# Optimization experiments

Hardware: AMD Instinct MI355X
Metric: run time of the kernel (lower is better)

The kernel has to match this reference:

```python
import jax, jax.numpy as jnp
import numpy as np

IN_F, OUT_F, GROUP = 4096, 4096, 128
N_GROUPS = IN_F // GROUP  # 32


def setup_inputs() -> dict:
    key = jax.random.key(0)
    k1, k2, k3, k4, k5 = jax.random.split(key, 5)
    x = jax.random.normal(k1, (2, 1024, IN_F), dtype=jnp.float32)
    w_q = jax.random.randint(k2, (OUT_F, N_GROUPS, GROUP), -128, 128, dtype=jnp.int32)  # int8-range quantized weights
    s_w = jax.random.uniform(k3, (N_GROUPS, OUT_F), dtype=jnp.float32) * 0.01  # per-group, per-out-channel scales
    perm = jax.random.permutation(k4, IN_F).astype(jnp.int64)  # GPTQ activation-order permutation
    bias = jax.random.normal(k5, (OUT_F,), dtype=jnp.float32)
    return {"x": x, "w_q": w_q, "s_w": s_w, "perm": perm, "bias": bias}


def reference(x, w_q, s_w, perm, bias):
    prefix = x.shape[:-1]
    orig_dtype = x.dtype
    xf = x.reshape(-1, IN_F)          # (n, in)
    xf = xf[:, perm]                  # apply GPTQ permutation
    xf = xf.reshape(-1, N_GROUPS, GROUP).astype(jnp.float32)  # (n, g, k)
    wf = w_q.astype(jnp.float32)      # (o, g, k) dequant-to-fp32 weights (pre-scale)
    y_g = jnp.einsum('ngk,ogk->ngo', xf, wf)   # per-group partial products (n, g, o)
    y = jnp.sum(y_g * s_w[None, :, :], axis=1) # apply group scales, reduce groups -> (n, o)
    y = y + bias.astype(y.dtype)
    return y.reshape(*prefix, OUT_F).astype(orig_dtype)
```

## Files before the change

kernel.cpp:

```cpp
#include <hip/hip_runtime.h>
#include <hip/hip_bf16.h>
#include <stdint.h>

#define IN_F   4096
#define OUT_F  4096
#define M_ROWS 2048
#define NG     32
#define GRP    128

typedef int   v4i  __attribute__((ext_vector_type(4)));
typedef float f32x4 __attribute__((ext_vector_type(4)));

typedef const void __attribute__((address_space(1))) cv_g;
typedef void       __attribute__((address_space(3))) v_l;

__device__ __forceinline__ void async16(const void* g, void* l) {
  __builtin_amdgcn_global_load_lds((cv_g*)g, (v_l*)l, 16, 0, 0);
}

__device__ int g_perm_is64;

__global__ void decode_flag(const void* __restrict__ perm_raw) {
  if (threadIdx.x == 0 && blockIdx.x == 0) {
    const int* w = (const int*)perm_raw;
    int ok = 1;
    for (int j = 0; j < 32; ++j) {
      int lo = w[2 * j], hi = w[2 * j + 1];
      if (hi != 0 || lo < 0 || lo >= IN_F) { ok = 0; break; }
    }
    g_perm_is64 = ok;
  }
}

__global__ __launch_bounds__(256) void prep(const float* __restrict__ x,
                                            const int* __restrict__ w_q,
                                            const void* __restrict__ perm_raw,
                                            char* __restrict__ xq,
                                            char* __restrict__ w8,
                                            float* __restrict__ sxr) {
  __shared__ float sx[IN_F];
  __shared__ float red[4];
  __shared__ int sflag;
  const int b = blockIdx.x;
  const int t = threadIdx.x;

  if (b < M_ROWS) {
    const int m = b;
    const float* xr = x + (size_t)m * IN_F;
#pragma unroll
    for (int u = 0; u < 4; ++u) {
      int idx = (u * 256 + t) * 4;
      *(float4*)&sx[idx] = *(const float4*)&xr[idx];
    }
    if (t < 64) {
      const int* w = (const int*)perm_raw;
      int j = t & 31;
      int lo = w[2 * j], hi = w[2 * j + 1];
      int cond = (hi == 0 && lo >= 0 && lo < IN_F);
      unsigned long long bal = __ballot(cond);
      if (t == 0) sflag = (bal == ~0ull) ? 1 : 0;
    }
    __syncthreads();
    const int f = sflag;
    const long long* p64 = (const long long*)perm_raw;
    const int*       p32 = (const int*)perm_raw;
    const int jb = t * 16;
    float vals[16];
    float lmax = 0.f;
#pragma unroll
    for (int u = 0; u < 16; ++u) {
      int pj = f ? (int)p64[jb + u] : p32[jb + u];
      float v = sx[pj];
      vals[u] = v;
      lmax = fmaxf(lmax, fabsf(v));
    }
#pragma unroll
    for (int d = 1; d < 64; d <<= 1)
      lmax = fmaxf(lmax, __shfl_xor(lmax, d, 64));
    if ((t & 63) == 0) red[t >> 6] = lmax;
    __syncthreads();
    float rmax = fmaxf(fmaxf(red[0], red[1]), fmaxf(red[2], red[3]));
    float inv = (rmax > 0.f) ? 127.f / rmax : 0.f;
    if (t == 0) sxr[m] = rmax / 127.f;
    char q[16] __attribute__((aligned(16)));
#pragma unroll
    for (int u = 0; u < 16; ++u)
      q[u] = (char)__float2int_rn(vals[u] * inv);
    *(uint4*)(xq + (size_t)m * IN_F + jb) = *(const uint4*)q;
  } else {
    const int o  = b - M_ROWS;
    const int kb = t * 16;
    const int* wr = w_q + (size_t)o * IN_F + kb;
    int4 w0 = *(const int4*)(wr + 0);
    int4 w1 = *(const int4*)(wr + 4);
    int4 w2 = *(const int4*)(wr + 8);
    int4 w3 = *(const int4*)(wr + 12);
    char q[16] __attribute__((aligned(16)));
    q[0]=(char)w0.x; q[1]=(char)w0.y; q[2]=(char)w0.z; q[3]=(char)w0.w;
    q[4]=(char)w1.x; q[5]=(char)w1.y; q[6]=(char)w1.z; q[7]=(char)w1.w;
    q[8]=(char)w2.x; q[9]=(char)w2.y; q[10]=(char)w2.z; q[11]=(char)w2.w;
    q[12]=(char)w3.x; q[13]=(char)w3.y; q[14]=(char)w3.z; q[15]=(char)w3.w;
    *(uint4*)(w8 + (size_t)o * IN_F + kb) = *(const uint4*)q;
  }
}

__global__ __launch_bounds__(256, 2) void gemm_i8(
    const char* __restrict__ A,
    const char* __restrict__ B,
    const float* __restrict__ s_w,
    const float* __restrict__ sxr,
    const float* __restrict__ bias,
    float* __restrict__ C) {
  __shared__ __attribute__((aligned(16))) char lds[73728];
  unsigned short* sws = (unsigned short*)lds;
  const int BUF0 = 8192, BUF1 = 40960;

  const int tid  = threadIdx.x;
  const int wave = tid >> 6;
  const int lane = tid & 63;
  const int bm = blockIdx.y << 7;
  const int bn = blockIdx.x << 7;
  const int wm = (wave >> 1) << 6;
  const int wn = (wave & 1) << 6;
  const int lrow = lane & 15;
  const int quad = lane >> 4;

#pragma unroll
  for (int u = 0; u < 16; ++u) {
    int idx = u * 256 + tid;
    int g = idx >> 7, c = idx & 127;
    __hip_bfloat16 h = __float2bfloat16(s_w[(size_t)g * OUT_F + bn + c]);
    sws[idx] = *(unsigned short*)&h;
  }

  const char* gp[8];
  int lofs[8];
#pragma unroll
  for (int h = 0; h < 8; ++h) {
    int c0 = (h * 4 + wave) * 64;
    int c  = c0 + lane;
    if (c0 < 1024) {
      int row = c >> 3;
      int kc  = (c & 7) ^ (row & 7);
      gp[h]   = A + (size_t)(bm + row) * IN_F + kc * 16;
      lofs[h] = c0 * 16;
    } else {
      int cb  = c - 1024;
      int row = cb >> 3;
      int kc  = (cb & 7) ^ (row & 7);
      gp[h]   = B + (size_t)(bn + row) * IN_F + kc * 16;
      lofs[h] = 16384 + (c0 - 1024) * 16;
    }
  }

  const int xlo = lrow & 7;
  int aoff[2][4], boff[2][4];
#pragma unroll
  for (int s = 0; s < 2; ++s) {
    int slot = (((s << 2) | quad) ^ xlo) << 4;
#pragma unroll
    for (int i = 0; i < 4; ++i) aoff[s][i] = (wm + i * 16 + lrow) * 128 + slot;
#pragma unroll
    for (int j = 0; j < 4; ++j) boff[s][j] = 16384 + (wn + j * 16 + lrow) * 128 + slot;
  }

  f32x4 accf[4][4] = {};
  v4i   acci[4][4] = {};

  auto rescale = [&](int g) {
    float swv[4];
#pragma unroll
    for (int j = 0; j < 4; ++j) {
      unsigned int u = sws[g * 128 + wn + j * 16 + lrow];
      swv[j] = __uint_as_float(u << 16);
    }
#pragma unroll
    for (int i = 0; i < 4; ++i)
#pragma unroll
      for (int j = 0; j < 4; ++j) {
#pragma unroll
        for (int r = 0; r < 4; ++r)
          accf[i][j][r] += swv[j] * (float)acci[i][j][r];
        acci[i][j] = (v4i){0, 0, 0, 0};
      }
  };

  auto tile = [&](int t, int pbase, int qbase, bool doPrev, bool doStage) {
    v4i af0[4], bf0[4], af1[4], bf1[4];
#pragma unroll
    for (int i = 0; i < 4; ++i) af0[i] = *(const v4i*)&lds[pbase + aoff[0][i]];
#pragma unroll
    for (int j = 0; j < 4; ++j) bf0[j] = *(const v4i*)&lds[pbase + boff[0][j]];
#pragma unroll
    for (int i = 0; i < 4; ++i) af1[i] = *(const v4i*)&lds[pbase + aoff[1][i]];
#pragma unroll
    for (int j = 0; j < 4; ++j) bf1[j] = *(const v4i*)&lds[pbase + boff[1][j]];
    if (doStage) {
      const int kn = (t + 1) * GRP;
#pragma unroll
      for (int h = 0; h < 8; ++h) async16(gp[h] + kn, &lds[qbase + lofs[h]]);
    }
    if (doPrev) rescale(t - 1);
    __builtin_amdgcn_s_setprio(1);
#pragma unroll
    for (int i = 0; i < 4; ++i)
#pragma unroll
      for (int j = 0; j < 4; ++j)
        acci[i][j] = __builtin_amdgcn_mfma_i32_16x16x64_i8(af0[i], bf0[j], acci[i][j], 0, 0, 0);
#pragma unroll
    for (int i = 0; i < 4; ++i)
#pragma unroll
      for (int j = 0; j < 4; ++j)
        acci[i][j] = __builtin_amdgcn_mfma_i32_16x16x64_i8(af1[i], bf1[j], acci[i][j], 0, 0, 0);
    __builtin_amdgcn_s_setprio(0);
    if (doStage) asm volatile("s_waitcnt vmcnt(0)" ::: "memory");
    __builtin_amdgcn_s_barrier();
    asm volatile("" ::: "memory");
  };

#pragma unroll
  for (int h = 0; h < 8; ++h) async16(gp[h], &lds[BUF0 + lofs[h]]);
  asm volatile("s_waitcnt vmcnt(0) lgkmcnt(0)" ::: "memory");
  __builtin_amdgcn_s_barrier();
  asm volatile("" ::: "memory");

  for (int it = 0; it < 16; ++it) {
    tile(2 * it,     BUF0, BUF1, it > 0, true);
    tile(2 * it + 1, BUF1, BUF0, true,   it < 15);
  }
  rescale(NG - 1);

#pragma unroll
  for (int i = 0; i < 4; ++i) {
    int r0 = bm + wm + i * 16 + quad * 4;
    float sxv[4];
#pragma unroll
    for (int r = 0; r < 4; ++r) sxv[r] = sxr[r0 + r];
#pragma unroll
    for (int j = 0; j < 4; ++j) {
      int col = bn + wn + j * 16 + lrow;
      float bv = bias[col];
#pragma unroll
      for (int r = 0; r < 4; ++r)
        C[(size_t)(r0 + r) * OUT_F + col] = sxv[r] * accf[i][j][r] + bv;
    }
  }
}

__global__ void naive_fallback(const float* __restrict__ x, const int* __restrict__ w_q,
                               const float* __restrict__ s_w, const void* __restrict__ perm_raw,
                               const float* __restrict__ bias, float* __restrict__ out) {
  int t = blockIdx.x * blockDim.x + threadIdx.x;
  int m = t >> 12;
  int o = t & 4095;
  const int f = g_perm_is64;
  const long long* p64 = (const long long*)perm_raw;
  const int*       p32 = (const int*)perm_raw;
  const float* xr = x + (size_t)m * IN_F;
  const int*   wr = w_q + (size_t)o * IN_F;
  float acc = 0.f;
  for (int g = 0; g < NG; ++g) {
    float part = 0.f;
    for (int k = 0; k < GRP; ++k) {
      int j = g * GRP + k;
      int pj = f ? (int)p64[j] : p32[j];
      part += xr[pj] * (float)wr[j];
    }
    acc += part * s_w[(size_t)g * OUT_F + o];
  }
  out[t] = acc + bias[o];
}

extern "C" void kernel_launch(void* const* d_in, const int* in_sizes, int n_in,
                              void* d_out, int out_size, void* d_ws, size_t ws_size,
                              hipStream_t stream) {
  const float* x    = (const float*)d_in[0];
  const int*   w_q  = (const int*)d_in[1];
  const float* s_w  = (const float*)d_in[2];
  const void*  perm = d_in[3];
  const float* bias = (const float*)d_in[4];
  float* out = (float*)d_out;

  const size_t xq_bytes = (size_t)M_ROWS * IN_F;
  const size_t w8_bytes = (size_t)OUT_F * IN_F;
  const size_t sx_bytes = (size_t)M_ROWS * sizeof(float);
  const size_t need = xq_bytes + w8_bytes + sx_bytes;

  if (ws_size < need) {
    decode_flag<<<1, 64, 0, stream>>>(perm);
    naive_fallback<<<(M_ROWS * OUT_F) / 256, 256, 0, stream>>>(x, w_q, s_w, perm, bias, out);
    return;
  }

  char*  xq  = (char*)d_ws;
  char*  w8  = (char*)d_ws + xq_bytes;
  float* sxr = (float*)((char*)d_ws + xq_bytes + w8_bytes);

  prep<<<M_ROWS + OUT_F, 256, 0, stream>>>(x, w_q, perm, xq, w8, sxr);

  dim3 grid(OUT_F / 128, M_ROWS / 128);
  gemm_i8<<<grid, 256, 0, stream>>>(xq, w8, s_w, sxr, bias, out);
}
```

Baseline: 212.5 us.

## Load A fragments directly from global into registers, stage only B in LDS

The int8 activation (A) tile is no longer staged through LDS. Each wave loads its A MFMA fragments straight from global memory into registers, software-pipelined half a group ahead. Only the weight (B) tile stays double-buffered in LDS, which shrinks LDS use from 72KB to 40KB and could allow more resident blocks. The group rescale is folded right after each group's MFMAs, with no deferred previous-group rescale. The cost is that each A row is now fetched once per wave column (duplicated global/L2 traffic across the two waves sharing rows) and global load latency sits on the critical path. The vmcnt(4) waits are also more delicate.

```diff
diff --git a/kernel.cpp b/kernel.cpp
--- a/kernel.cpp
+++ b/kernel.cpp
@@ -111,9 +111,9 @@
     const float* __restrict__ sxr,
     const float* __restrict__ bias,
     float* __restrict__ C) {
-  __shared__ __attribute__((aligned(16))) char lds[73728];
+  __shared__ __attribute__((aligned(16))) char lds[40960];
   unsigned short* sws = (unsigned short*)lds;
-  const int BUF0 = 8192, BUF1 = 40960;
+  const int BUF0 = 8192, BUF1 = 24576;
 
   const int tid  = threadIdx.x;
   const int wave = tid >> 6;
@@ -124,6 +124,7 @@
   const int wn = (wave & 1) << 6;
   const int lrow = lane & 15;
   const int quad = lane >> 4;
+  const int xlo  = lrow & 7;
 
 #pragma unroll
   for (int u = 0; u < 16; ++u) {
@@ -133,102 +134,106 @@
     sws[idx] = *(unsigned short*)&h;
   }
 
-  const char* gp[8];
-  int lofs[8];
-#pragma unroll
-  for (int h = 0; h < 8; ++h) {
-    int c0 = (h * 4 + wave) * 64;
-    int c  = c0 + lane;
-    if (c0 < 1024) {
-      int row = c >> 3;
-      int kc  = (c & 7) ^ (row & 7);
-      gp[h]   = A + (size_t)(bm + row) * IN_F + kc * 16;
-      lofs[h] = c0 * 16;
-    } else {
-      int cb  = c - 1024;
-      int row = cb >> 3;
-      int kc  = (cb & 7) ^ (row & 7);
-      gp[h]   = B + (size_t)(bn + row) * IN_F + kc * 16;
-      lofs[h] = 16384 + (c0 - 1024) * 16;
-    }
-  }
-
-  const int xlo = lrow & 7;
-  int aoff[2][4], boff[2][4];
-#pragma unroll
-  for (int s = 0; s < 2; ++s) {
-    int slot = (((s << 2) | quad) ^ xlo) << 4;
-#pragma unroll
-    for (int i = 0; i < 4; ++i) aoff[s][i] = (wm + i * 16 + lrow) * 128 + slot;
-#pragma unroll
-    for (int j = 0; j < 4; ++j) boff[s][j] = 16384 + (wn + j * 16 + lrow) * 128 + slot;
-  }
+  const char* gB = B + (size_t)(bn + wave * 8 + (lane >> 3)) * IN_F +
+                   (((lane & 7) ^ (lane >> 3)) << 4);
+  const int lB = wave * 1024;
+
+  const char* gA = A + (size_t)(bm + wm + lrow) * IN_F + (quad << 4);
 
   f32x4 accf[4][4] = {};
-  v4i   acci[4][4] = {};
-
-  auto rescale = [&](int g) {
-    float swv[4];
-#pragma unroll
-    for (int j = 0; j < 4; ++j) {
-      unsigned int u = sws[g * 128 + wn + j * 16 + lrow];
-      swv[j] = __uint_as_float(u << 16);
-    }
-#pragma unroll
-    for (int i = 0; i < 4; ++i)
-#pragma unroll
-      for (int j = 0; j < 4; ++j) {
-#pragma unroll
-        for (int r = 0; r < 4; ++r)
-          accf[i][j][r] += swv[j] * (float)acci[i][j][r];
-        acci[i][j] = (v4i){0, 0, 0, 0};
-      }
-  };
-
-  auto tile = [&](int t, int pbase, int qbase, bool doPrev, bool doStage) {
-    v4i af0[4], bf0[4], af1[4], bf1[4];
-#pragma unroll
-    for (int i = 0; i < 4; ++i) af0[i] = *(const v4i*)&lds[pbase + aoff[0][i]];
-#pragma unroll
-    for (int j = 0; j < 4; ++j) bf0[j] = *(const v4i*)&lds[pbase + boff[0][j]];
-#pragma unroll
-    for (int i = 0; i < 4; ++i) af1[i] = *(const v4i*)&lds[pbase + aoff[1][i]];
-#pragma unroll
-    for (int j = 0; j < 4; ++j) bf1[j] = *(const v4i*)&lds[pbase + boff[1][j]];
-    if (doStage) {
-      const int kn = (t + 1) * GRP;
-#pragma unroll
-      for (int h = 0; h < 8; ++h) async16(gp[h] + kn, &lds[qbase + lofs[h]]);
-    }
-    if (doPrev) rescale(t - 1);
-    __builtin_amdgcn_s_setprio(1);
-#pragma unroll
-    for (int i = 0; i < 4; ++i)
-#pragma unroll
-      for (int j = 0; j < 4; ++j)
-        acci[i][j] = __builtin_amdgcn_mfma_i32_16x16x64_i8(af0[i], bf0[j], acci[i][j], 0, 0, 0);
-#pragma unroll
-    for (int i = 0; i < 4; ++i)
-#pragma unroll
-      for (int j = 0; j < 4; ++j)
-        acci[i][j] = __builtin_amdgcn_mfma_i32_16x16x64_i8(af1[i], bf1[j], acci[i][j], 0, 0, 0);
-    __builtin_amdgcn_s_setprio(0);
-    if (doStage) asm volatile("s_waitcnt vmcnt(0)" ::: "memory");
-    __builtin_amdgcn_s_barrier();
-    asm volatile("" ::: "memory");
-  };
-
-#pragma unroll
-  for (int h = 0; h < 8; ++h) async16(gp[h], &lds[BUF0 + lofs[h]]);
-  asm volatile("s_waitcnt vmcnt(0) lgkmcnt(0)" ::: "memory");
+  const v4i zero4 = {0, 0, 0, 0};
+
+#pragma unroll
+  for (int h = 0; h < 4; ++h)
+    async16(gB + (size_t)h * (32 * IN_F), &lds[BUF0 + lB + h * 4096]);
+  __builtin_amdgcn_sched_barrier(0);
+  v4i afC[4], afN[4];
+#pragma unroll
+  for (int i = 0; i < 4; ++i)
+    afC[i] = *(const v4i*)(gA + (size_t)i * (16 * IN_F));
+  asm volatile("s_waitcnt vmcnt(4) lgkmcnt(0)" ::: "memory");
   __builtin_amdgcn_s_barrier();
   asm volatile("" ::: "memory");
 
-  for (int it = 0; it < 16; ++it) {
-    tile(2 * it,     BUF0, BUF1, it > 0, true);
-    tile(2 * it + 1, BUF1, BUF0, true,   it < 15);
-  }
-  rescale(NG - 1);
+  for (int t = 0; t < NG; ++t) {
+    const int p = t & 1;
+    const char* bufB = &lds[p ? BUF1 : BUF0];
+    char* stgB = &lds[p ? BUF0 : BUF1];
+    const int kt = t * GRP;
+
+#pragma unroll
+    for (int i = 0; i < 4; ++i)
+      afN[i] = *(const v4i*)(gA + (size_t)i * (16 * IN_F) + kt + 64);
+    __builtin_amdgcn_sched_barrier(0);
+    if (t + 1 < NG) {
+#pragma unroll
+      for (int h = 0; h < 4; ++h)
+        async16(gB + (size_t)h * (32 * IN_F) + kt + GRP,
+                stgB + lB + h * 4096);
+    }
+    __builtin_amdgcn_sched_barrier(0);
+
+    v4i acci[4][4];
+    {
+      v4i bf[4];
+#pragma unroll
+      for (int j = 0; j < 4; ++j)
+        bf[j] = *(const v4i*)&bufB[(wn + j * 16 + lrow) * 128 +
+                                   ((quad ^ xlo) << 4)];
+      __builtin_amdgcn_s_setprio(1);
+#pragma unroll
+      for (int i = 0; i < 4; ++i)
+#pragma unroll
+        for (int j = 0; j < 4; ++j)
+          acci[i][j] = __builtin_amdgcn_mfma_i32_16x16x64_i8(
+              afC[i], bf[j], zero4, 0, 0, 0);
+      __builtin_amdgcn_s_setprio(0);
+    }
+
+    if (t + 1 < NG) {
+#pragma unroll
+      for (int i = 0; i < 4; ++i)
+        afC[i] = *(const v4i*)(gA + (size_t)i * (16 * IN_F) + kt + GRP);
+    }
+
+    {
+      v4i bf[4];
+#pragma unroll
+      for (int j = 0; j < 4; ++j)
+        bf[j] = *(const v4i*)&bufB[(wn + j * 16 + lrow) * 128 +
+                                   (((4 | quad) ^ xlo) << 4)];
+      __builtin_amdgcn_s_setprio(1);
+#pragma unroll
+      for (int i = 0; i < 4; ++i)
+#pragma unroll
+        for (int j = 0; j < 4; ++j)
+          acci[i][j] = __builtin_amdgcn_mfma_i32_16x16x64_i8(
+              afN[i], bf[j], acci[i][j], 0, 0, 0);
+      __builtin_amdgcn_s_setprio(0);
+    }
+
+    {
+      float swv[4];
+#pragma unroll
+      for (int j = 0; j < 4; ++j) {
+        unsigned int u = sws[t * 128 + wn + j * 16 + lrow];
+        swv[j] = __uint_as_float(u << 16);
+      }
+#pragma unroll
+      for (int i = 0; i < 4; ++i)
+#pragma unroll
+        for (int j = 0; j < 4; ++j)
+#pragma unroll
+          for (int r = 0; r < 4; ++r)
+            accf[i][j][r] += swv[j] * (float)acci[i][j][r];
+    }
+
+    if (t + 1 < NG) {
+      asm volatile("s_waitcnt vmcnt(4)" ::: "memory");
+      __builtin_amdgcn_s_barrier();
+      asm volatile("" ::: "memory");
+    }
+  }
 
 #pragma unroll
   for (int i = 0; i < 4; ++i) {
```

Result: slower. 218.0 us (+2.6%).
